# Kernel tuning notes

Measured on AMD Instinct MI355X. Metric: run time of the kernel, lower is better.

## Reference

```python
import jax, jax.numpy as jnp
import numpy as np

SIZES = [8, 16, 32, 64, 128, 256]
C = 8
N = 2_000_000


def setup_inputs() -> dict:
    key = jax.random.key(0)
    ks = jax.random.split(key, len(SIZES) + 1)
    inp = {"t": jax.random.uniform(ks[0], (N, 1), dtype=jnp.float32)}
    for i, s in enumerate(SIZES):
        inp[f"vol{i}"] = jax.random.normal(ks[i + 1], (s, C), dtype=jnp.float32)
    return inp


def _interp(vol, tc):
    # vol: (size, c); tc: (N,) in [0, 1]
    # grid_sample(align_corners=True) with y = t*2-1 maps to pos = t*(size-1)
    size = vol.shape[0]
    pos = tc * (size - 1)
    i0 = jnp.clip(jnp.floor(pos).astype(jnp.int32), 0, size - 2)
    w = (pos - i0.astype(pos.dtype))[:, None]  # (N, 1)
    return vol[i0] * (1.0 - w) + vol[i0 + 1] * w  # (N, c)


def reference(t, vol0, vol1, vol2, vol3, vol4, vol5):
    tc = jnp.clip(t[:, 0], 0.0, 1.0)  # (N,)
    vols = (vol0, vol1, vol2, vol3, vol4, vol5)
    # concat per-level interpolated features -> (N, c * n_levels)
    return jnp.concatenate([_interp(v, tc) for v in vols], axis=-1)
```

## Files before the change

kernel.cpp:

```cpp
#include <hip/hip_runtime.h>


constexpr int NLEV = 6;
constexpr int CCH = 8;
constexpr int ROWS_TOTAL = 504;
constexpr int TILE = 256;
constexpr int F4_PER_ROW = 12;
constexpr int F4_PER_TILE = TILE * F4_PER_ROW;

__global__ __launch_bounds__(TILE) void interp_multires_kernel(
    const float* __restrict__ t,
    const float* __restrict__ v0, const float* __restrict__ v1,
    const float* __restrict__ v2, const float* __restrict__ v3,
    const float* __restrict__ v4, const float* __restrict__ v5,
    float* __restrict__ out, int n)
{
    __shared__ __align__(16) float vol_lds[ROWS_TOTAL * CCH];
    __shared__ float t_lds[TILE];

    const int tid = threadIdx.x;

    const float* vps[NLEV] = {v0, v1, v2, v3, v4, v5};
#pragma unroll
    for (int l = 0; l < NLEV; ++l) {
        const int sz = 8 << l;
        const int offf = (sz - 8) * CCH;
        const int n4 = sz * CCH / 4;
        float4* dst = (float4*)(vol_lds + offf);
        const float4* src = (const float4*)vps[l];
        for (int i = tid; i < n4; i += TILE) dst[i] = src[i];
    }

    {
        const int grow = blockIdx.x * TILE + tid;
        float tv = (grow < n) ? t[grow] : 0.0f;
        t_lds[tid] = fminf(fmaxf(tv, 0.0f), 1.0f);
    }
    __syncthreads();

    const long long base4 = (long long)blockIdx.x * F4_PER_TILE;
    float4* out4 = (float4*)out;
    const int row_base = blockIdx.x * TILE;

#pragma unroll
    for (int k = 0; k < F4_PER_ROW; ++k) {
        const int idx = k * TILE + tid;
        const int row = idx / F4_PER_ROW;
        const int q   = idx - row * F4_PER_ROW;
        if (row_base + row < n) {
            const int lvl = q >> 1;
            const int cb  = (q & 1) * 4;
            const int size = 8 << lvl;

            const float tc  = t_lds[row];
            const float pos = tc * (float)(size - 1);
            int i0 = (int)floorf(pos);
            i0 = min(max(i0, 0), size - 2);
            const float w  = pos - (float)i0;
            const float om = 1.0f - w;

            const float* p = vol_lds + ((size - 8) + i0) * CCH + cb;
            const float4 a = *(const float4*)p;
            const float4 b = *(const float4*)(p + CCH);

            float4 r;
            r.x = a.x * om + b.x * w;
            r.y = a.y * om + b.y * w;
            r.z = a.z * om + b.z * w;
            r.w = a.w * om + b.w * w;
            out4[base4 + idx] = r;
        }
    }
}

extern "C" void kernel_launch(void* const* d_in, const int* in_sizes, int n_in,
                              void* d_out, int out_size, void* d_ws, size_t ws_size,
                              hipStream_t stream) {
    const float* t  = (const float*)d_in[0];
    const float* v0 = (const float*)d_in[1];
    const float* v1 = (const float*)d_in[2];
    const float* v2 = (const float*)d_in[3];
    const float* v3 = (const float*)d_in[4];
    const float* v4 = (const float*)d_in[5];
    const float* v5 = (const float*)d_in[6];
    float* out = (float*)d_out;

    const int n = in_sizes[0];
    const int grid = (n + TILE - 1) / TILE;
    interp_multires_kernel<<<grid, TILE, 0, stream>>>(t, v0, v1, v2, v3, v4, v5,
                                                      out, n);
}
```

Before: 401.4 us.

## Use persistent grid-stride loop with nontemporal stores and direct t reads

Replaces the one-block-per-256-rows launch with a fixed 4096-block grid-stride loop over output float4s. Each block now loads the 504-row volume table into LDS once and reuses it across many tiles instead of once per tile. The t staging buffer is dropped; each thread reads t[row] straight from global memory, so 12 lanes read the same address. Output writes become nontemporal stores to avoid polluting cache with the 96 MB streaming output.

```diff
diff --git a/kernel.cpp b/kernel.cpp
--- a/kernel.cpp
+++ b/kernel.cpp
@@ -1,14 +1,15 @@
 #include <hip/hip_runtime.h>
 
+
+typedef float fx4 __attribute__((ext_vector_type(4)));
 
 constexpr int NLEV = 6;
 constexpr int CCH = 8;
 constexpr int ROWS_TOTAL = 504;
-constexpr int TILE = 256;
+constexpr int BLK = 256;
 constexpr int F4_PER_ROW = 12;
-constexpr int F4_PER_TILE = TILE * F4_PER_ROW;
 
-__global__ __launch_bounds__(TILE) void interp_multires_kernel(
+__global__ __launch_bounds__(BLK) void interp_multires_kernel(
     const float* __restrict__ t,
     const float* __restrict__ v0, const float* __restrict__ v1,
     const float* __restrict__ v2, const float* __restrict__ v3,
@@ -16,7 +17,6 @@
     float* __restrict__ out, int n)
 {
     __shared__ __align__(16) float vol_lds[ROWS_TOTAL * CCH];
-    __shared__ float t_lds[TILE];
 
     const int tid = threadIdx.x;
 
@@ -26,50 +26,36 @@
         const int sz = 8 << l;
         const int offf = (sz - 8) * CCH;
         const int n4 = sz * CCH / 4;
-        float4* dst = (float4*)(vol_lds + offf);
-        const float4* src = (const float4*)vps[l];
-        for (int i = tid; i < n4; i += TILE) dst[i] = src[i];
-    }
-
-    {
-        const int grow = blockIdx.x * TILE + tid;
-        float tv = (grow < n) ? t[grow] : 0.0f;
-        t_lds[tid] = fminf(fmaxf(tv, 0.0f), 1.0f);
+        fx4* dst = (fx4*)(vol_lds + offf);
+        const fx4* src = (const fx4*)vps[l];
+        for (int i = tid; i < n4; i += BLK) dst[i] = src[i];
     }
     __syncthreads();
 
-    const long long base4 = (long long)blockIdx.x * F4_PER_TILE;
-    float4* out4 = (float4*)out;
-    const int row_base = blockIdx.x * TILE;
+    const int total4 = n * F4_PER_ROW;
+    const int stride = gridDim.x * BLK;
+    fx4* __restrict__ out4 = (fx4*)out;
 
-#pragma unroll
-    for (int k = 0; k < F4_PER_ROW; ++k) {
-        const int idx = k * TILE + tid;
-        const int row = idx / F4_PER_ROW;
-        const int q   = idx - row * F4_PER_ROW;
-        if (row_base + row < n) {
-            const int lvl = q >> 1;
-            const int cb  = (q & 1) * 4;
-            const int size = 8 << lvl;
+    for (int g = blockIdx.x * BLK + tid; g < total4; g += stride) {
+        const int row = g / F4_PER_ROW;
+        const int q   = g - row * F4_PER_ROW;
+        const int lvl = q >> 1;
+        const int cb  = (q & 1) * 4;
+        const int size = 8 << lvl;
 
-            const float tc  = t_lds[row];
-            const float pos = tc * (float)(size - 1);
-            int i0 = (int)floorf(pos);
-            i0 = min(max(i0, 0), size - 2);
-            const float w  = pos - (float)i0;
-            const float om = 1.0f - w;
+        const float tc  = fminf(fmaxf(t[row], 0.0f), 1.0f);
+        const float pos = tc * (float)(size - 1);
+        int i0 = (int)floorf(pos);
+        i0 = min(max(i0, 0), size - 2);
+        const float w  = pos - (float)i0;
+        const float om = 1.0f - w;
 
-            const float* p = vol_lds + ((size - 8) + i0) * CCH + cb;
-            const float4 a = *(const float4*)p;
-            const float4 b = *(const float4*)(p + CCH);
+        const float* p = vol_lds + ((size - 8) + i0) * CCH + cb;
+        const fx4 a = *(const fx4*)p;
+        const fx4 b = *(const fx4*)(p + CCH);
 
-            float4 r;
-            r.x = a.x * om + b.x * w;
-            r.y = a.y * om + b.y * w;
-            r.z = a.z * om + b.z * w;
-            r.w = a.w * om + b.w * w;
-            out4[base4 + idx] = r;
-        }
+        const fx4 r = a * om + b * w;
+        __builtin_nontemporal_store(r, out4 + g);
     }
 }
 
@@ -86,7 +72,10 @@
     float* out = (float*)d_out;
 
     const int n = in_sizes[0];
-    const int grid = (n + TILE - 1) / TILE;
-    interp_multires_kernel<<<grid, TILE, 0, stream>>>(t, v0, v1, v2, v3, v4, v5,
-                                                      out, n);
+    const int total4 = n * F4_PER_ROW;
+    int grid = 4096;
+    const int max_grid = (total4 + BLK - 1) / BLK;
+    if (grid > max_grid) grid = max_grid;
+    interp_multires_kernel<<<grid, BLK, 0, stream>>>(t, v0, v1, v2, v3, v4, v5,
+                                                     out, n);
 }
```

Result: no change. 401.2 us (-0.0%).
